# Kernel tuning notes

Measured on AMD Instinct MI355X. Metric: run time of the kernel, lower is better.

Reference implementation:

```python
import jax, jax.numpy as jnp
import numpy as np

V, TB, L, H, D, HD, FF = 50257, 1024, 6, 12, 768, 64, 4 * 768
B, T = 2, 1024
EOS = 50256


def _layernorm(x, g, b, eps=1e-5):
    mu = x.mean(-1, keepdims=True)
    var = ((x - mu) ** 2).mean(-1, keepdims=True)
    return (x - mu) * jax.lax.rsqrt(var + eps) * g + b


def setup_inputs() -> dict:
    key = jax.random.key(0)
    ks = jax.random.split(key, 10)
    resid_std = 0.02 * (2 * L) ** (-0.5)

    def n(k, shape, std=0.02):
        return (std * jax.random.normal(k, shape)).astype(jnp.float32)

    return {
        "idx": jax.random.randint(ks[0], (B, T), 0, V, dtype=jnp.int32),
        "targets": jax.random.randint(ks[1], (B, T), 0, V, dtype=jnp.int32),
        "token_emb": n(ks[2], (V, D)),           # tied with head
        "pos_emb": n(ks[3], (1, TB, D)),
        "ln1_g": jnp.ones((L, D), jnp.float32),
        "ln1_b": jnp.zeros((L, D), jnp.float32),
        "ln2_g": jnp.ones((L, D), jnp.float32),
        "ln2_b": jnp.zeros((L, D), jnp.float32),
        "W_qkv": n(ks[4], (L, D, 3 * D)),
        "b_qkv": jnp.zeros((L, 3 * D), jnp.float32),
        "W_proj": n(ks[5], (L, D, D), resid_std),
        "b_proj": jnp.zeros((L, D), jnp.float32),
        "W_fc1": n(ks[6], (L, D, FF)),
        "b_fc1": jnp.zeros((L, FF), jnp.float32),
        "W_fc2": n(ks[7], (L, FF, D), resid_std),
        "b_fc2": jnp.zeros((L, D), jnp.float32),
        "lnf_g": jnp.ones((D,), jnp.float32),
        "lnf_b": jnp.zeros((D,), jnp.float32),
    }


def reference(idx, targets, token_emb, pos_emb, ln1_g, ln1_b, ln2_g, ln2_b,
              W_qkv, b_qkv, W_proj, b_proj, W_fc1, b_fc1, W_fc2, b_fc2,
              lnf_g, lnf_b):
    Bc, Tc = idx.shape
    x = token_emb[idx] + pos_emb[:, :Tc, :]  # [B,T,D]; dropout=0 -> identity

    # document-boundary causal mask: same_doc & causal
    is_eos = (idx == EOS).astype(jnp.int32)
    doc_id = jnp.cumsum(is_eos, axis=1) - is_eos          # [B,T]
    same_doc = doc_id[:, :, None] == doc_id[:, None, :]   # [B,T,T]
    causal = jnp.tril(jnp.ones((Tc, Tc), dtype=bool))
    mask = same_doc & causal                               # [B,T,T]
    scale = 1.0 / float(np.sqrt(HD))

    def block(x, p):
        g1, b1, Wq, bq, Wp, bp, g2, b2, Wf1, bf1, Wf2, bf2 = p
        h = _layernorm(x, g1, b1)
        qkv = (h @ Wq + bq).reshape(Bc, Tc, 3, H, HD)
        q = qkv[:, :, 0].transpose(0, 2, 1, 3)  # [B,H,T,hd]
        k = qkv[:, :, 1].transpose(0, 2, 1, 3)
        v = qkv[:, :, 2].transpose(0, 2, 1, 3)
        att = jnp.einsum('bhqd,bhkd->bhqk', q, k) * scale
        att = jnp.where(mask[:, None, :, :], att, -jnp.inf)
        att = jax.nn.softmax(att, axis=-1)
        y = jnp.einsum('bhqk,bhkd->bhqd', att, v)
        y = y.transpose(0, 2, 1, 3).reshape(Bc, Tc, D)
        x = x + (y @ Wp + bp)
        h2 = _layernorm(x, g2, b2)
        x = x + (jax.nn.gelu(h2 @ Wf1 + bf1, approximate=False) @ Wf2 + bf2)
        return x, None

    x, _ = jax.lax.scan(block, x, (ln1_g, ln1_b, W_qkv, b_qkv, W_proj, b_proj,
                                   ln2_g, ln2_b, W_fc1, b_fc1, W_fc2, b_fc2))
    x = _layernorm(x, lnf_g, lnf_b)
    logits = x @ token_emb.T  # tied head, no bias
    logp = jax.nn.log_softmax(logits, axis=-1)
    tgt = targets.astype(jnp.int32)[..., None]
    loss = -jnp.take_along_axis(logp, tgt, axis=-1).mean()
    return logits, loss
```

## Files before the change

kernel.cpp:

```cpp
#include <hip/hip_runtime.h>
#include <hip/hip_bf16.h>
#include <math.h>

#define V_ 50257
#define L_ 6
#define H_ 12
#define D_ 768
#define HD_ 64
#define FF_ 3072
#define B_ 2
#define T_ 1024
#define NTOK (B_*T_)
#define EOS_ 50256
#define QBLK 64
#define KVB 64
#define NS2 393
#define QS3 (3*D_)

typedef __attribute__((ext_vector_type(8))) short s16x8;
typedef __attribute__((ext_vector_type(4))) float f32x4;

__device__ __forceinline__ short f2bf(float f) {
  __hip_bfloat16 h = __float2bfloat16(f);
  return *reinterpret_cast<short*>(&h);
}

__device__ __forceinline__ void gl_lds16(const void* g, void* l) {
  __builtin_amdgcn_global_load_lds(
      (const __attribute__((address_space(1))) unsigned int*)g,
      (__attribute__((address_space(3))) unsigned int*)l, 16, 0, 0);
}

__global__ void k_embed(const int* __restrict__ idx, const float* __restrict__ tok,
                        const float* __restrict__ pos, float* __restrict__ x) {
  int gid = blockIdx.x * blockDim.x + threadIdx.x;
  const int total = NTOK * D_;
  if (gid >= total) return;
  int row = gid / D_;
  int d = gid - row * D_;
  int t = row & (T_ - 1);
  x[gid] = tok[(size_t)idx[row] * D_ + d] + pos[t * D_ + d];
}

__global__ void k_docid(const int* __restrict__ idx, int* __restrict__ doc) {
  int b = threadIdx.x;
  if (b >= B_) return;
  int c = 0;
  for (int t = 0; t < T_; ++t) {
    int e = (idx[b*T_ + t] == EOS_) ? 1 : 0;
    doc[b*T_ + t] = c;
    c += e;
  }
}

__global__ void k_cast_tok(const float* __restrict__ in,
                           __hip_bfloat16* __restrict__ out, long n8) {
  long i = (long)blockIdx.x*blockDim.x + threadIdx.x;
  long stride = (long)gridDim.x*blockDim.x;
  for (; i < n8; i += stride) {
    const float4* src = (const float4*)(in + i*8);
    float4 v0 = src[0], v1 = src[1];
    s16x8 s;
    s[0]=f2bf(v0.x); s[1]=f2bf(v0.y); s[2]=f2bf(v0.z); s[3]=f2bf(v0.w);
    s[4]=f2bf(v1.x); s[5]=f2bf(v1.y); s[6]=f2bf(v1.z); s[7]=f2bf(v1.w);
    *(s16x8*)((short*)out + i*8) = s;
  }
}

__global__ void k_ln(const float* __restrict__ x, const float* __restrict__ g,
                     const float* __restrict__ b, __hip_bfloat16* __restrict__ out) {
  int row = blockIdx.x;
  const float* xr = x + (size_t)row * D_;
  int lane = threadIdx.x;
  float vals[D_/64];
  float s = 0.f;
  #pragma unroll
  for (int i = 0; i < D_/64; ++i) { vals[i] = xr[lane + i*64]; s += vals[i]; }
  #pragma unroll
  for (int o = 1; o < 64; o <<= 1) s += __shfl_xor(s, o);
  float mu = s * (1.f/D_);
  float v = 0.f;
  #pragma unroll
  for (int i = 0; i < D_/64; ++i) { float d0 = vals[i]-mu; v += d0*d0; }
  #pragma unroll
  for (int o = 1; o < 64; o <<= 1) v += __shfl_xor(v, o);
  float inv = rsqrtf(v * (1.f/D_) + 1e-5f);
  #pragma unroll
  for (int i = 0; i < D_/64; ++i) {
    int d = lane + i*64;
    out[(size_t)row*D_ + d] = __float2bfloat16((vals[i]-mu)*inv*g[d] + b[d]);
  }
}

__global__ void k_wt(const float* __restrict__ in, __hip_bfloat16* __restrict__ out,
                     int K, int N) {
  __shared__ float tile[32][33];
  int l = blockIdx.z;
  const float* src = in + (size_t)l*K*N;
  __hip_bfloat16* dst = out + (size_t)l*N*K;
  int n0 = blockIdx.x*32, k0 = blockIdx.y*32;
  int tx = threadIdx.x, ty = threadIdx.y;
  #pragma unroll
  for (int i = 0; i < 4; ++i)
    tile[ty + i*8][tx] = src[(size_t)(k0 + ty + i*8)*N + n0 + tx];
  __syncthreads();
  #pragma unroll
  for (int i = 0; i < 4; ++i)
    dst[(size_t)(n0 + ty + i*8)*K + k0 + tx] = __float2bfloat16(tile[tx][ty + i*8]);
}

__global__ __launch_bounds__(512) void k_mfma_nt(
    const __hip_bfloat16* __restrict__ A,
    const __hip_bfloat16* __restrict__ Bh,
    const float* __restrict__ Bf,
    const float* __restrict__ bias,
    const float* resid,
    float* outf, __hip_bfloat16* outh,
    int M, int N, int K, int gelu)
{
  __shared__ __align__(16) short lds_a[2][128*64];
  __shared__ __align__(16) short lds_b[2][128*64];
  const int t = threadIdx.x;
  const int m0 = blockIdx.y * 128;
  const int n0 = blockIdx.x * 128;
  const int lane = t & 63;
  const int wid = t >> 6;
  const int wm = (wid >> 2) * 64;
  const int wn = (wid & 3) * 32;
  const int lrow = lane & 15;
  const int lkb = (lane >> 4) * 16;
  const int wbase = (t & 448) * 16;

  auto stageA = [&](int buf, int k0) {
    #pragma unroll
    for (int p = 0; p < 2; ++p) {
      int c = p*512 + t;
      int row = c >> 3;
      int colb = (c & 7) << 4;
      const char* src = (const char*)A + ((size_t)(m0+row)*K + k0)*2 + (colb ^ ((row & 7) << 4));
      gl_lds16(src, (char*)lds_a[buf] + p*8192 + wbase);
    }
  };
  auto stageB = [&](int buf, int k0) {
    if (Bh) {
      #pragma unroll
      for (int p = 0; p < 2; ++p) {
        int c = p*512 + t;
        int row = c >> 3;
        int colb = (c & 7) << 4;
        const char* src = (const char*)Bh + ((size_t)(n0+row)*K + k0)*2 + (colb ^ ((row & 7) << 4));
        gl_lds16(src, (char*)lds_b[buf] + p*8192 + wbase);
      }
    } else {
      #pragma unroll
      for (int p = 0; p < 2; ++p) {
        int c = p*512 + t;
        int row = c >> 3;
        int colb = (c & 7) << 4;
        int gn = n0 + row;
        s16x8 s = {0,0,0,0,0,0,0,0};
        if (gn < N) {
          const char* src = (const char*)Bf + ((size_t)gn*K + k0)*4 + colb*2;
          float4 v0 = *(const float4*)src;
          float4 v1 = *(const float4*)(src + 16);
          s[0]=f2bf(v0.x); s[1]=f2bf(v0.y); s[2]=f2bf(v0.z); s[3]=f2bf(v0.w);
          s[4]=f2bf(v1.x); s[5]=f2bf(v1.y); s[6]=f2bf(v1.z); s[7]=f2bf(v1.w);
        }
        int dst = (row*128 + colb) ^ ((row & 7) << 4);
        *(s16x8*)((char*)lds_b[buf] + dst) = s;
      }
    }
  };

  f32x4 acc[4][2];
  #pragma unroll
  for (int i = 0; i < 4; ++i)
    #pragma unroll
    for (int j = 0; j < 2; ++j)
      acc[i][j] = (f32x4){0.f, 0.f, 0.f, 0.f};

  const int nk = K >> 6;
  stageA(0, 0); stageB(0, 0);
  stageA(1, 64); stageB(1, 64);
  const bool piped = (Bh != nullptr);
  for (int kt = 0; kt < nk; ++kt) {
    if (piped && kt + 1 < nk) asm volatile("s_waitcnt vmcnt(4)" ::: "memory");
    else                      asm volatile("s_waitcnt vmcnt(0) lgkmcnt(0)" ::: "memory");
    __builtin_amdgcn_s_barrier();
    const int cur = kt & 1;
    #pragma unroll
    for (int ks = 0; ks < 2; ++ks) {
      s16x8 af[4], bfr[2];
      #pragma unroll
      for (int f = 0; f < 4; ++f) {
        int row = wm + f*16 + lrow;
        int off = (row*128 + ks*64 + lkb) ^ ((row & 7) << 4);
        af[f] = *(const s16x8*)((const char*)lds_a[cur] + off);
      }
      #pragma unroll
      for (int f = 0; f < 2; ++f) {
        int row = wn + f*16 + lrow;
        int off = (row*128 + ks*64 + lkb) ^ ((row & 7) << 4);
        bfr[f] = *(const s16x8*)((const char*)lds_b[cur] + off);
      }
      #pragma unroll
      for (int fm = 0; fm < 4; ++fm)
        #pragma unroll
        for (int fn = 0; fn < 2; ++fn)
          acc[fm][fn] = __builtin_amdgcn_mfma_f32_16x16x32_bf16(
              af[fm], bfr[fn], acc[fm][fn], 0, 0, 0);
    }
    __builtin_amdgcn_s_barrier();
    if (kt + 2 < nk) { stageA(cur, (kt+2)*64); stageB(cur, (kt+2)*64); }
  }
  const int crow = (lane >> 4) * 4;
  #pragma unroll
  for (int fm = 0; fm < 4; ++fm) {
    #pragma unroll
    for (int fn = 0; fn < 2; ++fn) {
      int col = n0 + wn + fn*16 + lrow;
      if (col >= N) continue;
      #pragma unroll
      for (int r = 0; r < 4; ++r) {
        int row = m0 + wm + fm*16 + crow + r;
        float v = acc[fm][fn][r];
        if (bias) v += bias[col];
        if (gelu) v = 0.5f * v * (1.f + erff(v * 0.70710678118654752f));
        if (resid) v += resid[(size_t)row*N + col];
        if (outf) outf[(size_t)row*N + col] = v;
        else      outh[(size_t)row*N + col] = __float2bfloat16(v);
      }
    }
  }
}

__global__ __launch_bounds__(256) void k_mfma_nt64(
    const __hip_bfloat16* __restrict__ A,
    const __hip_bfloat16* __restrict__ Bh,
    const float* __restrict__ bias,
    const float* resid,
    float* outf,
    int M, int N, int K)
{
  __shared__ __align__(16) short lds_a[64*64];
  __shared__ __align__(16) short lds_b[64*64];
  const int t = threadIdx.x;
  const int m0 = blockIdx.y * 64;
  const int n0 = blockIdx.x * 64;
  const int lane = t & 63;
  const int wid = t >> 6;
  const int wm = (wid >> 1) * 32;
  const int wn = (wid & 1) * 32;
  const int lrow = lane & 15;
  const int lkb = (lane >> 4) * 16;
  const int wbase = (t & 192) * 16;

  f32x4 acc[2][2];
  #pragma unroll
  for (int i = 0; i < 2; ++i)
    #pragma unroll
    for (int j = 0; j < 2; ++j)
      acc[i][j] = (f32x4){0.f, 0.f, 0.f, 0.f};

  for (int k0 = 0; k0 < K; k0 += 64) {
    #pragma unroll
    for (int p = 0; p < 2; ++p) {
      int c = p*256 + t;
      int row = c >> 3;
      int colb = (c & 7) << 4;
      const char* srcA = (const char*)A + ((size_t)(m0+row)*K + k0)*2 + (colb ^ ((row & 7) << 4));
      gl_lds16(srcA, (char*)lds_a + p*4096 + wbase);
    }
    #pragma unroll
    for (int p = 0; p < 2; ++p) {
      int c = p*256 + t;
      int row = c >> 3;
      int colb = (c & 7) << 4;
      const char* srcB = (const char*)Bh + ((size_t)(n0+row)*K + k0)*2 + (colb ^ ((row & 7) << 4));
      gl_lds16(srcB, (char*)lds_b + p*4096 + wbase);
    }
    __syncthreads();
    #pragma unroll
    for (int ks = 0; ks < 2; ++ks) {
      s16x8 af[2], bfr[2];
      #pragma unroll
      for (int f = 0; f < 2; ++f) {
        int row = wm + f*16 + lrow;
        int off = (row*128 + ks*64 + lkb) ^ ((row & 7) << 4);
        af[f] = *(const s16x8*)((const char*)lds_a + off);
      }
      #pragma unroll
      for (int f = 0; f < 2; ++f) {
        int row = wn + f*16 + lrow;
        int off = (row*128 + ks*64 + lkb) ^ ((row & 7) << 4);
        bfr[f] = *(const s16x8*)((const char*)lds_b + off);
      }
      #pragma unroll
      for (int fm = 0; fm < 2; ++fm)
        #pragma unroll
        for (int fn = 0; fn < 2; ++fn)
          acc[fm][fn] = __builtin_amdgcn_mfma_f32_16x16x32_bf16(
              af[fm], bfr[fn], acc[fm][fn], 0, 0, 0);
    }
    __syncthreads();
  }
  const int crow = (lane >> 4) * 4;
  #pragma unroll
  for (int fm = 0; fm < 2; ++fm) {
    #pragma unroll
    for (int fn = 0; fn < 2; ++fn) {
      int col = n0 + wn + fn*16 + lrow;
      #pragma unroll
      for (int r = 0; r < 4; ++r) {
        int row = m0 + wm + fm*16 + crow + r;
        float v = acc[fm][fn][r] + bias[col];
        if (resid) v += resid[(size_t)row*N + col];
        outf[(size_t)row*N + col] = v;
      }
    }
  }
}

__global__ __launch_bounds__(512) void k_logits(
    const __hip_bfloat16* __restrict__ A,
    const __hip_bfloat16* __restrict__ Bh,
    const float* __restrict__ Bf,
    float* __restrict__ C,
    float2* __restrict__ part)
{
  __shared__ __align__(16) short lds_a[2][128*64];
  __shared__ __align__(16) short lds_b[2][128*64];
  const int t = threadIdx.x;
  const int bid = blockIdx.x;
  const int lid = (bid & 7) * (NS2*16/8) + (bid >> 3);
  const int m0 = (lid & 15) * 128;
  const int nt = lid >> 4;
  const int n0 = nt * 128;
  const int lane = t & 63;
  const int wid = t >> 6;
  const int wm = (wid >> 2) * 64;
  const int wn = (wid & 3) * 32;
  const int lrow = lane & 15;
  const int lkb = (lane >> 4) * 16;
  const int wbase = (t & 448) * 16;

  auto stageA = [&](int buf, int k0) {
    #pragma unroll
    for (int p = 0; p < 2; ++p) {
      int c = p*512 + t;
      int row = c >> 3;
      int colb = (c & 7) << 4;
      const char* src = (const char*)A + ((size_t)(m0+row)*768 + k0)*2 + (colb ^ ((row & 7) << 4));
      gl_lds16(src, (char*)lds_a[buf] + p*8192 + wbase);
    }
  };
  auto stageB = [&](int buf, int k0) {
    if (Bh) {
      #pragma unroll
      for (int p = 0; p < 2; ++p) {
        int c = p*512 + t;
        int row = c >> 3;
        int colb = (c & 7) << 4;
        const char* src = (const char*)Bh + ((size_t)(n0+row)*768 + k0)*2 + (colb ^ ((row & 7) << 4));
        gl_lds16(src, (char*)lds_b[buf] + p*8192 + wbase);
      }
    } else {
      #pragma unroll
      for (int p = 0; p < 2; ++p) {
        int c = p*512 + t;
        int row = c >> 3;
        int colb = (c & 7) << 4;
        int gn = n0 + row;
        s16x8 s = {0,0,0,0,0,0,0,0};
        if (gn < V_) {
          const char* src = (const char*)Bf + ((size_t)gn*768 + k0)*4 + colb*2;
          float4 v0 = *(const float4*)src;
          float4 v1 = *(const float4*)(src + 16);
          s[0]=f2bf(v0.x); s[1]=f2bf(v0.y); s[2]=f2bf(v0.z); s[3]=f2bf(v0.w);
          s[4]=f2bf(v1.x); s[5]=f2bf(v1.y); s[6]=f2bf(v1.z); s[7]=f2bf(v1.w);
        }
        int dst = (row*128 + colb) ^ ((row & 7) << 4);
        *(s16x8*)((char*)lds_b[buf] + dst) = s;
      }
    }
  };

  f32x4 acc[4][2];
  #pragma unroll
  for (int i = 0; i < 4; ++i)
    #pragma unroll
    for (int j = 0; j < 2; ++j)
      acc[i][j] = (f32x4){0.f, 0.f, 0.f, 0.f};

  stageA(0, 0); stageB(0, 0);
  stageA(1, 64); stageB(1, 64);
  const bool piped = (Bh != nullptr);
  for (int kt = 0; kt < 12; ++kt) {
    if (piped && kt + 1 < 12) asm volatile("s_waitcnt vmcnt(4)" ::: "memory");
    else                      asm volatile("s_waitcnt vmcnt(0) lgkmcnt(0)" ::: "memory");
    __builtin_amdgcn_s_barrier();
    const int cur = kt & 1;
    #pragma unroll
    for (int ks = 0; ks < 2; ++ks) {
      s16x8 af[4], bfr[2];
      #pragma unroll
      for (int f = 0; f < 4; ++f) {
        int row = wm + f*16 + lrow;
        int off = (row*128 + ks*64 + lkb) ^ ((row & 7) << 4);
        af[f] = *(const s16x8*)((const char*)lds_a[cur] + off);
      }
      #pragma unroll
      for (int f = 0; f < 2; ++f) {
        int row = wn + f*16 + lrow;
        int off = (row*128 + ks*64 + lkb) ^ ((row & 7) << 4);
        bfr[f] = *(const s16x8*)((const char*)lds_b[cur] + off);
      }
      #pragma unroll
      for (int fm = 0; fm < 4; ++fm)
        #pragma unroll
        for (int fn = 0; fn < 2; ++fn)
          acc[fm][fn] = __builtin_amdgcn_mfma_f32_16x16x32_bf16(
              af[fm], bfr[fn], acc[fm][fn], 0, 0, 0);
    }
    __builtin_amdgcn_s_barrier();
    if (kt + 2 < 12) { stageA(cur, (kt+2)*64); stageB(cur, (kt+2)*64); }
  }
  const int crow = (lane >> 4) * 4;
  bool valid[2];
  #pragma unroll
  for (int fn = 0; fn < 2; ++fn) valid[fn] = (n0 + wn + fn*16 + lrow) < V_;
  float2* red = (float2*)lds_a;
  #pragma unroll
  for (int fm = 0; fm < 4; ++fm) {
    #pragma unroll
    for (int r = 0; r < 4; ++r) {
      int rit = wm + fm*16 + crow + r;
      int row = m0 + rit;
      float m = -1e30f;
      #pragma unroll
      for (int fn = 0; fn < 2; ++fn) {
        if (valid[fn]) {
          float v = acc[fm][fn][r];
          C[(size_t)row*V_ + n0 + wn + fn*16 + lrow] = v;
          m = fmaxf(m, v);
        }
      }
      #pragma unroll
      for (int o = 1; o < 16; o <<= 1) m = fmaxf(m, __shfl_xor(m, o));
      float s = 0.f;
      #pragma unroll
      for (int fn = 0; fn < 2; ++fn)
        if (valid[fn]) s += __expf(acc[fm][fn][r] - m);
      #pragma unroll
      for (int o = 1; o < 16; o <<= 1) s += __shfl_xor(s, o);
      if (lrow == 0) red[rit*4 + (wid & 3)] = make_float2(m, s);
    }
  }
  __syncthreads();
  if (t < 128) {
    float M = -1e30f, S = 0.f;
    #pragma unroll
    for (int wc = 0; wc < 4; ++wc) {
      float2 p = red[t*4 + wc];
      float mn = fmaxf(M, p.x);
      S = S*__expf(M - mn) + p.y*__expf(p.x - mn);
      M = mn;
    }
    part[(size_t)(m0 + t)*NS2 + nt] = make_float2(M, S);
  }
}

__global__ void k_rowloss2(const float2* __restrict__ part,
                           const float* __restrict__ logits,
                           const int* __restrict__ tgt, float* __restrict__ rl) {
  int row = blockIdx.x;
  int lane = threadIdx.x;
  float M = -1e30f, S = 0.f;
  for (int i = lane; i < NS2; i += 64) {
    float2 p = part[(size_t)row*NS2 + i];
    float mn = fmaxf(M, p.x);
    S = S*__expf(M - mn) + p.y*__expf(p.x - mn);
    M = mn;
  }
  #pragma unroll
  for (int o = 1; o < 64; o <<= 1) {
    float Mo = __shfl_xor(M, o);
    float So = __shfl_xor(S, o);
    float mn = fmaxf(M, Mo);
    S = S*__expf(M - mn) + So*__expf(Mo - mn);
    M = mn;
  }
  if (lane == 0)
    rl[row] = (logf(S) + M) - logits[(size_t)row*V_ + tgt[row]];
}

__global__ __launch_bounds__(256) void k_fattn(
    const __hip_bfloat16* __restrict__ qkv, const int* __restrict__ doc,
    __hip_bfloat16* __restrict__ y)
{
  __shared__ __align__(16) short q_lds[QBLK*64];
  __shared__ __align__(16) short k_lds[KVB*64];
  __shared__ __align__(16) short vt_lds[64*KVB];
  __shared__ __align__(16) short p_lds[4][16*64];
  __shared__ int doc_k[KVB];
  const int t = threadIdx.x;
  const int lane = t & 63;
  const int w = t >> 6;
  const int q0 = (gridDim.x - 1 - blockIdx.x) * QBLK;
  const int h = blockIdx.y, b = blockIdx.z;
  const int lrow = lane & 15;
  const int lgrp = lane >> 4;
  const int crow = lgrp * 4;
  const int wbase = (t & 192) * 16;
  const short* qp = (const short*)qkv;

  #pragma unroll
  for (int p = 0; p < 2; ++p) {
    int c = p*256 + t;
    int row = c >> 3;
    int colb = (c & 7) << 4;
    const char* src = (const char*)(qp + ((size_t)(b*T_ + q0 + row))*QS3 + h*HD_)
                      + (colb ^ ((row & 7) << 4));
    gl_lds16(src, (char*)q_lds + p*4096 + wbase);
  }
  int docq[4];
  #pragma unroll
  for (int r = 0; r < 4; ++r)
    docq[r] = doc[b*T_ + q0 + w*16 + crow + r];
  __syncthreads();

  float m_r[4], l_r[4];
  #pragma unroll
  for (int r = 0; r < 4; ++r) { m_r[r] = -1e30f; l_r[r] = 0.f; }
  f32x4 o[4];
  #pragma unroll
  for (int fd = 0; fd < 4; ++fd) o[fd] = (f32x4){0.f,0.f,0.f,0.f};

  const int ntiles = q0/KVB + 1;
  for (int kt = 0; kt < ntiles; ++kt) {
    const int kv0 = kt * KVB;
    #pragma unroll
    for (int p = 0; p < 2; ++p) {
      int c = p*256 + t;
      int row = c >> 3;
      int colb = (c & 7) << 4;
      const char* src = (const char*)(qp + ((size_t)(b*T_ + kv0 + row))*QS3 + D_ + h*HD_)
                        + (colb ^ ((row & 7) << 4));
      gl_lds16(src, (char*)k_lds + p*4096 + wbase);
    }
    #pragma unroll
    for (int p = 0; p < 2; ++p) {
      int c = p*256 + t;
      int kvr = c >> 3, d0 = (c & 7)*8;
      s16x8 s = *(const s16x8*)(qp + ((size_t)(b*T_ + kv0 + kvr))*QS3 + 2*D_ + h*HD_ + d0);
      #pragma unroll
      for (int j = 0; j < 8; ++j) {
        int d = d0 + j;
        int off = (d*128 + kvr*2) ^ ((d & 7) << 4);
        *(short*)((char*)vt_lds + off) = s[j];
      }
    }
    if (t < KVB) doc_k[t] = doc[b*T_ + kv0 + t];
    __syncthreads();

    f32x4 sfr[4];
    #pragma unroll
    for (int fn = 0; fn < 4; ++fn) sfr[fn] = (f32x4){0.f,0.f,0.f,0.f};
    #pragma unroll
    for (int ks = 0; ks < 2; ++ks) {
      int arow = w*16 + lrow;
      s16x8 af = *(const s16x8*)((const char*)q_lds +
                 ((arow*128 + lgrp*16 + ks*64) ^ ((arow & 7) << 4)));
      #pragma unroll
      for (int fn = 0; fn < 4; ++fn) {
        int brow = fn*16 + lrow;
        s16x8 bf = *(const s16x8*)((const char*)k_lds +
                   ((brow*128 + lgrp*16 + ks*64) ^ ((brow & 7) << 4)));
        sfr[fn] = __builtin_amdgcn_mfma_f32_16x16x32_bf16(af, bf, sfr[fn], 0, 0, 0);
      }
    }
    int dk[4];
    #pragma unroll
    for (int fn = 0; fn < 4; ++fn) dk[fn] = doc_k[fn*16 + lrow];
    float rowmax[4] = {-1e30f, -1e30f, -1e30f, -1e30f};
    #pragma unroll
    for (int fn = 0; fn < 4; ++fn) {
      int col = kv0 + fn*16 + lrow;
      #pragma unroll
      for (int r = 0; r < 4; ++r) {
        int qrow = q0 + w*16 + crow + r;
        bool ok = (col <= qrow) && (dk[fn] == docq[r]);
        float v = ok ? sfr[fn][r] * 0.125f : -1e30f;
        sfr[fn][r] = v;
        rowmax[r] = fmaxf(rowmax[r], v);
      }
    }
    #pragma unroll
    for (int r = 0; r < 4; ++r) {
      float v = rowmax[r];
      #pragma unroll
      for (int off = 1; off < 16; off <<= 1) v = fmaxf(v, __shfl_xor(v, off));
      rowmax[r] = v;
    }
    float alpha[4], psum[4];
    #pragma unroll
    for (int r = 0; r < 4; ++r) {
      float mn = fmaxf(m_r[r], rowmax[r]);
      alpha[r] = __expf(m_r[r] - mn);
      m_r[r] = mn;
      psum[r] = 0.f;
    }
    #pragma unroll
    for (int fn = 0; fn < 4; ++fn) {
      #pragma unroll
      for (int r = 0; r < 4; ++r) {
        float sv = sfr[fn][r];
        float p = (sv < -5e29f) ? 0.f : __expf(sv - m_r[r]);
        psum[r] += p;
        int rl_ = crow + r;
        int off = (rl_*128 + (fn*16 + lrow)*2) ^ ((rl_ & 7) << 4);
        *(short*)((char*)p_lds[w] + off) = f2bf(p);
      }
    }
    #pragma unroll
    for (int r = 0; r < 4; ++r) {
      float v = psum[r];
      #pragma unroll
      for (int off = 1; off < 16; off <<= 1) v += __shfl_xor(v, off);
      l_r[r] = l_r[r]*alpha[r] + v;
    }
    #pragma unroll
    for (int fd = 0; fd < 4; ++fd)
      #pragma unroll
      for (int r = 0; r < 4; ++r)
        o[fd][r] *= alpha[r];
    #pragma unroll
    for (int ks = 0; ks < 2; ++ks) {
      s16x8 af = *(const s16x8*)((const char*)p_lds[w] +
                 ((lrow*128 + lgrp*16 + ks*64) ^ ((lrow & 7) << 4)));
      #pragma unroll
      for (int fd = 0; fd < 4; ++fd) {
        int brow = fd*16 + lrow;
        s16x8 bf = *(const s16x8*)((const char*)vt_lds +
                   ((brow*128 + lgrp*16 + ks*64) ^ ((brow & 7) << 4)));
        o[fd] = __builtin_amdgcn_mfma_f32_16x16x32_bf16(af, bf, o[fd], 0, 0, 0);
      }
    }
    __syncthreads();
  }
  #pragma unroll
  for (int r = 0; r < 4; ++r) {
    float inv = 1.f / l_r[r];
    int rowg = b*T_ + q0 + w*16 + crow + r;
    #pragma unroll
    for (int fd = 0; fd < 4; ++fd) {
      int col = h*HD_ + fd*16 + lrow;
      y[(size_t)rowg*D_ + col] = __float2bfloat16(o[fd][r] * inv);
    }
  }
}

__global__ void k_rowloss(const float* __restrict__ logits,
                          const int* __restrict__ tgt, float* __restrict__ rl) {
  __shared__ float red[4];
  int row = blockIdx.x;
  const float* lr = logits + (size_t)row * V_;
  int tid = threadIdx.x;
  float m = -1e30f;
  for (int v = tid; v < V_; v += 256) m = fmaxf(m, lr[v]);
  #pragma unroll
  for (int o = 1; o < 64; o <<= 1) m = fmaxf(m, __shfl_xor(m, o));
  if ((tid & 63) == 0) red[tid >> 6] = m;
  __syncthreads();
  m = fmaxf(fmaxf(red[0], red[1]), fmaxf(red[2], red[3]));
  __syncthreads();
  float s = 0.f;
  for (int v = tid; v < V_; v += 256) s += __expf(lr[v] - m);
  #pragma unroll
  for (int o = 1; o < 64; o <<= 1) s += __shfl_xor(s, o);
  if ((tid & 63) == 0) red[tid >> 6] = s;
  __syncthreads();
  if (tid == 0) {
    s = red[0]+red[1]+red[2]+red[3];
    rl[row] = (logf(s) + m) - lr[tgt[row]];
  }
}

__global__ void k_loss(const float* __restrict__ rl, float* __restrict__ out) {
  __shared__ float red[4];
  int tid = threadIdx.x;
  float s = 0.f;
  for (int i = tid; i < NTOK; i += 256) s += rl[i];
  #pragma unroll
  for (int o = 1; o < 64; o <<= 1) s += __shfl_xor(s, o);
  if ((tid & 63) == 0) red[tid >> 6] = s;
  __syncthreads();
  if (tid == 0) {
    s = red[0]+red[1]+red[2]+red[3];
    out[0] = s / (float)NTOK;
  }
}

extern "C" void kernel_launch(void* const* d_in, const int* in_sizes, int n_in,
                              void* d_out, int out_size, void* d_ws, size_t ws_size,
                              hipStream_t stream) {
  const int*   idx   = (const int*)d_in[0];
  const int*   tgt   = (const int*)d_in[1];
  const float* tok   = (const float*)d_in[2];
  const float* pos   = (const float*)d_in[3];
  const float* ln1_g = (const float*)d_in[4];
  const float* ln1_b = (const float*)d_in[5];
  const float* ln2_g = (const float*)d_in[6];
  const float* ln2_b = (const float*)d_in[7];
  const float* W_qkv = (const float*)d_in[8];
  const float* b_qkv = (const float*)d_in[9];
  const float* W_proj= (const float*)d_in[10];
  const float* b_proj= (const float*)d_in[11];
  const float* W_fc1 = (const float*)d_in[12];
  const float* b_fc1 = (const float*)d_in[13];
  const float* W_fc2 = (const float*)d_in[14];
  const float* b_fc2 = (const float*)d_in[15];
  const float* lnf_g = (const float*)d_in[16];
  const float* lnf_b = (const float*)d_in[17];

  float* out = (float*)d_out;

  char* ob = (char*)d_out;
  float*           x    = (float*)(ob + 0);
  __hip_bfloat16*  qkv  = (__hip_bfloat16*)(ob + (size_t)6291456);
  __hip_bfloat16*  y    = (__hip_bfloat16*)(ob + (size_t)15728640);
  __hip_bfloat16*  tff  = (__hip_bfloat16*)(ob + (size_t)18874368);
  __hip_bfloat16*  WTq  = (__hip_bfloat16*)(ob + (size_t)40894464);
  __hip_bfloat16*  WTp  = (__hip_bfloat16*)(ob + (size_t)62128128);
  __hip_bfloat16*  WT1  = (__hip_bfloat16*)(ob + (size_t)69206016);
  __hip_bfloat16*  WT2  = (__hip_bfloat16*)(ob + (size_t)97517568);

  char* wb = (char*)d_ws;
  __hip_bfloat16* h    = (__hip_bfloat16*)(wb + 0);
  int*    doc  = (int*)  (wb + (size_t)3145728);
  float*  rl   = (float*)(wb + (size_t)3153920);
  float2* part = (float2*)(wb + (size_t)3162112);
  __hip_bfloat16* tokh = (__hip_bfloat16*)(wb + (size_t)9601024);
  const size_t ws_need_part = (size_t)9601024;
  const size_t ws_need_tokh = (size_t)9601024 + 77194752 + 131072;
  const bool fused_loss = (ws_size >= ws_need_part);
  const bool use_tokh   = (ws_size >= ws_need_tokh);

  dim3 tb(32, 8);
  k_wt<<<dim3(2304/32, 768/32, L_), tb, 0, stream>>>(W_qkv,  WTq,  768, 2304);
  k_wt<<<dim3( 768/32, 768/32, L_), tb, 0, stream>>>(W_proj, WTp,  768,  768);
  k_wt<<<dim3(3072/32, 768/32, L_), tb, 0, stream>>>(W_fc1,  WT1,  768, 3072);
  k_wt<<<dim3( 768/32,3072/32, L_), tb, 0, stream>>>(W_fc2,  WT2, 3072,  768);
  if (use_tokh)
    k_cast_tok<<<2048, 256, 0, stream>>>(tok, tokh, (long)V_*768/8);

  k_embed<<<(NTOK*D_ + 255)/256, 256, 0, stream>>>(idx, tok, pos, x);
  k_docid<<<1, 64, 0, stream>>>(idx, doc);

  for (int l = 0; l < L_; ++l) {
    k_ln<<<NTOK, 64, 0, stream>>>(x, ln1_g + l*D_, ln1_b + l*D_, h);
    k_mfma_nt<<<dim3(2304/128, NTOK/128), 512, 0, stream>>>(
        h, WTq + (size_t)l*2304*768, nullptr, b_qkv + (size_t)l*2304, nullptr,
        nullptr, qkv, NTOK, 2304, 768, 0);
    k_fattn<<<dim3(T_/QBLK, H_, B_), 256, 0, stream>>>(qkv, doc, y);
    k_mfma_nt64<<<dim3(768/64, NTOK/64), 256, 0, stream>>>(
        y, WTp + (size_t)l*768*768, b_proj + (size_t)l*768, x, x,
        NTOK, 768, 768);
    k_ln<<<NTOK, 64, 0, stream>>>(x, ln2_g + l*D_, ln2_b + l*D_, h);
    k_mfma_nt<<<dim3(3072/128, NTOK/128), 512, 0, stream>>>(
        h, WT1 + (size_t)l*3072*768, nullptr, b_fc1 + (size_t)l*3072, nullptr,
        nullptr, tff, NTOK, 3072, 768, 1);
    k_mfma_nt64<<<dim3(768/64, NTOK/64), 256, 0, stream>>>(
        tff, WT2 + (size_t)l*768*3072, b_fc2 + (size_t)l*768, x, x,
        NTOK, 768, 3072);
  }
  k_ln<<<NTOK, 64, 0, stream>>>(x, lnf_g, lnf_b, h);

  if (fused_loss) {
    k_logits<<<NS2*16, 512, 0, stream>>>(
        h, use_tokh ? tokh : nullptr, tok, out, part);
    k_rowloss2<<<NTOK, 64, 0, stream>>>(part, out, tgt, rl);
  } else {
    k_mfma_nt<<<dim3((V_ + 127)/128, NTOK/128), 512, 0, stream>>>(
        h, nullptr, tok, nullptr, nullptr, out, nullptr, NTOK, V_, 768, 0);
    k_rowloss<<<NTOK, 256, 0, stream>>>(out, tgt, rl);
  }
  k_loss<<<1, 256, 0, stream>>>(rl, out + (size_t)NTOK*V_);
}
```

Baseline: 1.528 ms.

## Double M tile of logits GEMM to 256 rows to reuse B tile

```diff
diff --git a/kernel.cpp b/kernel.cpp
--- a/kernel.cpp
+++ b/kernel.cpp
@@ -328,13 +328,15 @@
     float* __restrict__ C,
     float2* __restrict__ part)
 {
-  __shared__ __align__(16) short lds_a[2][128*64];
-  __shared__ __align__(16) short lds_b[2][128*64];
+  __shared__ __align__(16) short lds_a0[2][128*64];
+  __shared__ __align__(16) short lds_a1[2][128*64];
+  __shared__ __align__(16) short lds_b [2][128*64];
   const int t = threadIdx.x;
   const int bid = blockIdx.x;
-  const int lid = (bid & 7) * (NS2*16/8) + (bid >> 3);
-  const int m0 = (lid & 15) * 128;
-  const int nt = lid >> 4;
+  const int lid = (bid & 7) * NS2 + (bid >> 3);
+  const int mg = lid & 7;
+  const int nt = lid >> 3;
+  const int m0 = mg * 256;
   const int n0 = nt * 128;
   const int lane = t & 63;
   const int wid = t >> 6;
@@ -344,25 +346,26 @@
   const int lkb = (lane >> 4) * 16;
   const int wbase = (t & 448) * 16;
 
-  auto stageA = [&](int buf, int k0) {
+  auto stage = [&](int buf, int k0) {
     #pragma unroll
     for (int p = 0; p < 2; ++p) {
       int c = p*512 + t;
       int row = c >> 3;
       int colb = (c & 7) << 4;
-      const char* src = (const char*)A + ((size_t)(m0+row)*768 + k0)*2 + (colb ^ ((row & 7) << 4));
-      gl_lds16(src, (char*)lds_a[buf] + p*8192 + wbase);
-    }
-  };
-  auto stageB = [&](int buf, int k0) {
+      int sw = colb ^ ((row & 7) << 4);
+      gl_lds16((const char*)A + ((size_t)(m0+row)*768 + k0)*2 + sw,
+               (char*)lds_a0[buf] + p*8192 + wbase);
+      gl_lds16((const char*)A + ((size_t)(m0+128+row)*768 + k0)*2 + sw,
+               (char*)lds_a1[buf] + p*8192 + wbase);
+    }
     if (Bh) {
       #pragma unroll
       for (int p = 0; p < 2; ++p) {
         int c = p*512 + t;
         int row = c >> 3;
         int colb = (c & 7) << 4;
-        const char* src = (const char*)Bh + ((size_t)(n0+row)*768 + k0)*2 + (colb ^ ((row & 7) << 4));
-        gl_lds16(src, (char*)lds_b[buf] + p*8192 + wbase);
+        gl_lds16((const char*)Bh + ((size_t)(n0+row)*768 + k0)*2 + (colb ^ ((row & 7) << 4)),
+                 (char*)lds_b[buf] + p*8192 + wbase);
       }
     } else {
       #pragma unroll
@@ -385,29 +388,32 @@
     }
   };
 
-  f32x4 acc[4][2];
+  f32x4 acc0[4][2], acc1[4][2];
   #pragma unroll
   for (int i = 0; i < 4; ++i)
     #pragma unroll
-    for (int j = 0; j < 2; ++j)
-      acc[i][j] = (f32x4){0.f, 0.f, 0.f, 0.f};
-
-  stageA(0, 0); stageB(0, 0);
-  stageA(1, 64); stageB(1, 64);
+    for (int j = 0; j < 2; ++j) {
+      acc0[i][j] = (f32x4){0.f, 0.f, 0.f, 0.f};
+      acc1[i][j] = (f32x4){0.f, 0.f, 0.f, 0.f};
+    }
+
+  stage(0, 0);
+  stage(1, 64);
   const bool piped = (Bh != nullptr);
   for (int kt = 0; kt < 12; ++kt) {
-    if (piped && kt + 1 < 12) asm volatile("s_waitcnt vmcnt(4)" ::: "memory");
+    if (piped && kt + 1 < 12) asm volatile("s_waitcnt vmcnt(6)" ::: "memory");
     else                      asm volatile("s_waitcnt vmcnt(0) lgkmcnt(0)" ::: "memory");
     __builtin_amdgcn_s_barrier();
     const int cur = kt & 1;
     #pragma unroll
     for (int ks = 0; ks < 2; ++ks) {
-      s16x8 af[4], bfr[2];
+      s16x8 af0[4], af1[4], bfr[2];
       #pragma unroll
       for (int f = 0; f < 4; ++f) {
         int row = wm + f*16 + lrow;
         int off = (row*128 + ks*64 + lkb) ^ ((row & 7) << 4);
-        af[f] = *(const s16x8*)((const char*)lds_a[cur] + off);
+        af0[f] = *(const s16x8*)((const char*)lds_a0[cur] + off);
+        af1[f] = *(const s16x8*)((const char*)lds_a1[cur] + off);
       }
       #pragma unroll
       for (int f = 0; f < 2; ++f) {
@@ -418,46 +424,52 @@
       #pragma unroll
       for (int fm = 0; fm < 4; ++fm)
         #pragma unroll
-        for (int fn = 0; fn < 2; ++fn)
-          acc[fm][fn] = __builtin_amdgcn_mfma_f32_16x16x32_bf16(
-              af[fm], bfr[fn], acc[fm][fn], 0, 0, 0);
+        for (int fn = 0; fn < 2; ++fn) {
+          acc0[fm][fn] = __builtin_amdgcn_mfma_f32_16x16x32_bf16(
+              af0[fm], bfr[fn], acc0[fm][fn], 0, 0, 0);
+          acc1[fm][fn] = __builtin_amdgcn_mfma_f32_16x16x32_bf16(
+              af1[fm], bfr[fn], acc1[fm][fn], 0, 0, 0);
+        }
     }
     __builtin_amdgcn_s_barrier();
-    if (kt + 2 < 12) { stageA(cur, (kt+2)*64); stageB(cur, (kt+2)*64); }
+    if (kt + 2 < 12) stage(cur, (kt+2)*64);
   }
   const int crow = (lane >> 4) * 4;
   bool valid[2];
   #pragma unroll
   for (int fn = 0; fn < 2; ++fn) valid[fn] = (n0 + wn + fn*16 + lrow) < V_;
-  float2* red = (float2*)lds_a;
-  #pragma unroll
-  for (int fm = 0; fm < 4; ++fm) {
-    #pragma unroll
-    for (int r = 0; r < 4; ++r) {
-      int rit = wm + fm*16 + crow + r;
-      int row = m0 + rit;
-      float m = -1e30f;
-      #pragma unroll
-      for (int fn = 0; fn < 2; ++fn) {
-        if (valid[fn]) {
-          float v = acc[fm][fn][r];
-          C[(size_t)row*V_ + n0 + wn + fn*16 + lrow] = v;
-          m = fmaxf(m, v);
+  float2* red = (float2*)lds_a0;
+  #pragma unroll
+  for (int set = 0; set < 2; ++set) {
+    #pragma unroll
+    for (int fm = 0; fm < 4; ++fm) {
+      #pragma unroll
+      for (int r = 0; r < 4; ++r) {
+        int rit = wm + fm*16 + crow + r;
+        int row = m0 + set*128 + rit;
+        float m = -1e30f;
+        #pragma unroll
+        for (int fn = 0; fn < 2; ++fn) {
+          if (valid[fn]) {
+            float v = set ? acc1[fm][fn][r] : acc0[fm][fn][r];
+            C[(size_t)row*V_ + n0 + wn + fn*16 + lrow] = v;
+            m = fmaxf(m, v);
+          }
         }
-      }
-      #pragma unroll
-      for (int o = 1; o < 16; o <<= 1) m = fmaxf(m, __shfl_xor(m, o));
-      float s = 0.f;
-      #pragma unroll
-      for (int fn = 0; fn < 2; ++fn)
-        if (valid[fn]) s += __expf(acc[fm][fn][r] - m);
-      #pragma unroll
-      for (int o = 1; o < 16; o <<= 1) s += __shfl_xor(s, o);
-      if (lrow == 0) red[rit*4 + (wid & 3)] = make_float2(m, s);
+        #pragma unroll
+        for (int o = 1; o < 16; o <<= 1) m = fmaxf(m, __shfl_xor(m, o));
+        float s = 0.f;
+        #pragma unroll
+        for (int fn = 0; fn < 2; ++fn)
+          if (valid[fn]) s += __expf((set ? acc1[fm][fn][r] : acc0[fm][fn][r]) - m);
+        #pragma unroll
+        for (int o = 1; o < 16; o <<= 1) s += __shfl_xor(s, o);
+        if (lrow == 0) red[(set*128 + rit)*4 + (wid & 3)] = make_float2(m, s);
+      }
     }
   }
   __syncthreads();
-  if (t < 128) {
+  if (t < 256) {
     float M = -1e30f, S = 0.f;
     #pragma unroll
     for (int wc = 0; wc < 4; ++wc) {
@@ -777,7 +789,7 @@
   k_ln<<<NTOK, 64, 0, stream>>>(x, lnf_g, lnf_b, h);
 
   if (fused_loss) {
-    k_logits<<<NS2*16, 512, 0, stream>>>(
+    k_logits<<<NS2*8, 512, 0, stream>>>(
         h, use_tokh ? tokh : nullptr, tok, out, part);
     k_rowloss2<<<NTOK, 64, 0, stream>>>(part, out, tgt, rl);
   } else {
```

After: 1.605 ms. 1.05x slower.
